# Kernel tuning notes

Measured on AMD Instinct MI355X. Metric: run time of the kernel, lower is better.

Reference implementation:

```python
import jax, jax.numpy as jnp
import numpy as np

TOP_K = 2
NUM_EXPERTS = 64
TEMPERATURE = 3.0           # buffer initial value (moe_routing_temperature default)
LOAD_BALANCE_ALPHA = 0.01
Z_LOSS_ALPHA = 1e-4


def setup_inputs() -> dict:
    key = jax.random.key(0)
    k1, k2 = jax.random.split(key)
    B, S, H, E = 4, 4096, 4096, NUM_EXPERTS
    x = jax.random.normal(k1, (B, S, H), dtype=jnp.float32)
    gate_w = jax.random.normal(k2, (E, H), dtype=jnp.float32) * (1.0 / np.sqrt(H))
    expert_bias = jnp.zeros((E,), dtype=jnp.float32)
    return {"x": x, "gate_w": gate_w, "expert_bias": expert_bias}


def reference(x, gate_w, expert_bias):
    # Eval-mode path: no noise, no warmup scaling, static top_k, seq_len < 8192
    # -> logits scaled by the temperature buffer.
    B, S, H = x.shape
    E = gate_w.shape[0]
    x_flat = x.reshape(-1, H)                               # [T, H], T = B*S
    logits = jnp.einsum('th,eh->te', x_flat, gate_w) + expert_bias  # [T, E]
    logits = logits / TEMPERATURE
    probs = jax.nn.softmax(logits, axis=-1)                 # [T, E]
    top_scores, top_idx = jax.lax.top_k(probs, TOP_K)       # [T, K]
    top_scores = top_scores / jnp.sum(top_scores, axis=-1, keepdims=True)
    # Load-balance aux loss: fraction of routed tokens per expert * mean prob.
    sel_counts = jax.nn.one_hot(top_idx, E, dtype=logits.dtype).sum(axis=1)  # [T, E]
    frac_routed = sel_counts.mean(axis=0)                   # [E], sums to TOP_K
    mean_prob = probs.mean(axis=0)                          # [E]
    lb_loss = LOAD_BALANCE_ALPHA * E * jnp.sum(frac_routed * mean_prob)
    # Z-loss for routing stability.
    z_loss = Z_LOSS_ALPHA * jnp.mean(jax.nn.logsumexp(logits, axis=-1) ** 2)
    total_loss = lb_loss + z_loss
    return top_scores, top_idx, total_loss
```

## Files before the change

kernel.cpp:

```cpp
#include <hip/hip_runtime.h>
#include <hip/hip_bf16.h>
#include <math.h>

typedef float f32x4 __attribute__((ext_vector_type(4)));

#define H_DIM   4096
#define E_EXP   64
#define NTOK    16384
#define BT      64
#define BK      64
#define LDX     68
#define NBLK    (NTOK/BT)
#define PART_STRIDE 132

__global__ __launch_bounds__(256) void moe_gate_main(
    const float* __restrict__ x, const float* __restrict__ gw,
    const float* __restrict__ bias, float* __restrict__ out,
    float* __restrict__ part)
{
    __shared__ float xs[BT * LDX];
    __shared__ float ws[E_EXP * LDX];
    __shared__ float bs[E_EXP];
    __shared__ float rs[BT];
    __shared__ int   ia[BT], ib[BT];

    const int tid  = threadIdx.x;
    const int bid  = blockIdx.x;
    const int tok0 = bid * BT;
    const int tx   = tid & 15;
    const int ty   = tid >> 4;

    if (tid < E_EXP) bs[tid] = bias[tid];

    const int srow = tid >> 4;
    const int scol = (tid & 15) * 4;
    const float* xp = x  + (size_t)(tok0 + srow) * H_DIM + scol;
    const float* wp = gw + (size_t)srow * H_DIM + scol;

    float acc[4][4];
#pragma unroll
    for (int i = 0; i < 4; i++)
#pragma unroll
        for (int j = 0; j < 4; j++) acc[i][j] = 0.f;

    f32x4 rx[4], rw[4];
#pragma unroll
    for (int i = 0; i < 4; i++) {
        rx[i] = *(const f32x4*)(xp + (size_t)(16 * i) * H_DIM);
        rw[i] = *(const f32x4*)(wp + (size_t)(16 * i) * H_DIM);
    }

    for (int c = 0; c < H_DIM / BK; c++) {
        __syncthreads();
#pragma unroll
        for (int i = 0; i < 4; i++) {
            *(f32x4*)&xs[(srow + 16 * i) * LDX + scol] = rx[i];
            *(f32x4*)&ws[(srow + 16 * i) * LDX + scol] = rw[i];
        }
        __syncthreads();
        if (c + 1 < H_DIM / BK) {
            const int k0 = (c + 1) * BK;
#pragma unroll
            for (int i = 0; i < 4; i++) {
                rx[i] = *(const f32x4*)(xp + (size_t)(16 * i) * H_DIM + k0);
                rw[i] = *(const f32x4*)(wp + (size_t)(16 * i) * H_DIM + k0);
            }
        }
#pragma unroll
        for (int kk = 0; kk < BK; kk += 4) {
            f32x4 xv[4], wv[4];
#pragma unroll
            for (int i = 0; i < 4; i++) xv[i] = *(const f32x4*)&xs[(ty + 16 * i) * LDX + kk];
#pragma unroll
            for (int j = 0; j < 4; j++) wv[j] = *(const f32x4*)&ws[(tx + 16 * j) * LDX + kk];
#pragma unroll
            for (int i = 0; i < 4; i++)
#pragma unroll
                for (int j = 0; j < 4; j++)
#pragma unroll
                    for (int q = 0; q < 4; q++)
                        acc[i][j] += xv[i][q] * wv[j][q];
        }
    }

    __syncthreads();
#pragma unroll
    for (int i = 0; i < 4; i++)
#pragma unroll
        for (int j = 0; j < 4; j++)
            xs[(ty + 16 * i) * LDX + (tx + 16 * j)] = acc[i][j];
    __syncthreads();

    float zsq = 0.f;
    if (tid < BT) {
        const float invTemp = (1.0f / 3.0f);
        float m = -1e30f, m2 = -1e30f;
        int i1 = 0, i2 = 0;
        for (int e = 0; e < E_EXP; e++) {
            float v = (xs[tid * LDX + e] + bs[e]) * invTemp;
            xs[tid * LDX + e] = v;
            if (v > m)       { m2 = m; i2 = i1; m = v; i1 = e; }
            else if (v > m2) { m2 = v; i2 = e; }
        }
        float s = 0.f;
        for (int e = 0; e < E_EXP; e++) {
            float p = expf(xs[tid * LDX + e] - m);
            xs[tid * LDX + e] = p;
            s += p;
        }
        rs[tid] = 1.0f / s;
        ia[tid] = i1; ib[tid] = i2;

        float p2   = expf(m2 - m);
        float inv12 = 1.0f / (1.0f + p2);
        out[(size_t)(tok0 + tid) * 2 + 0] = inv12;
        out[(size_t)(tok0 + tid) * 2 + 1] = p2 * inv12;
        out[(size_t)NTOK * 2 + (size_t)(tok0 + tid) * 2 + 0] = (float)i1;
        out[(size_t)NTOK * 2 + (size_t)(tok0 + tid) * 2 + 1] = (float)i2;

        float lse = m + logf(s);
        zsq = lse * lse;
#pragma unroll
        for (int o = 32; o; o >>= 1) zsq += __shfl_xor(zsq, o);
    }
    __syncthreads();

    if (tid < E_EXP) {
        float psum = 0.f, csum = 0.f;
        for (int t = 0; t < BT; t++) {
            psum += xs[t * LDX + tid] * rs[t];
            csum += (ia[t] == tid ? 1.f : 0.f) + (ib[t] == tid ? 1.f : 0.f);
        }
        part[bid * PART_STRIDE + tid]      = psum;
        part[bid * PART_STRIDE + 64 + tid] = csum;
        if (tid == 0) part[bid * PART_STRIDE + 128] = zsq;
    }
}

__global__ void moe_gate_loss(const float* __restrict__ part, float* __restrict__ out)
{
    const int tid = threadIdx.x;
    float sp = 0.f, sc = 0.f, zp = 0.f;
    for (int b = 0; b < NBLK; b++) {
        sp += part[b * PART_STRIDE + tid];
        sc += part[b * PART_STRIDE + 64 + tid];
    }
    for (int m = 0; m < NBLK / 64; m++)
        zp += part[(tid + 64 * m) * PART_STRIDE + 128];

    const float invN = 1.0f / (float)NTOK;
    float dot = (sc * invN) * (sp * invN);
#pragma unroll
    for (int o = 32; o; o >>= 1) {
        dot += __shfl_xor(dot, o);
        zp  += __shfl_xor(zp, o);
    }
    if (tid == 0)
        out[(size_t)NTOK * 4] = 0.01f * 64.0f * dot + 1e-4f * zp * invN;
}

extern "C" void kernel_launch(void* const* d_in, const int* in_sizes, int n_in,
                              void* d_out, int out_size, void* d_ws, size_t ws_size,
                              hipStream_t stream)
{
    const float* x    = (const float*)d_in[0];
    const float* gw   = (const float*)d_in[1];
    const float* bias = (const float*)d_in[2];
    float* out  = (float*)d_out;
    float* part = (float*)d_ws;

    moe_gate_main<<<NBLK, 256, 0, stream>>>(x, gw, bias, out, part);
    moe_gate_loss<<<1, 64, 0, stream>>>(part, out);
}
```

Baseline: 477.4 us.

## Replace FP32 SIMT gate GEMM with split-bf16 MFMA emulation and parallel loss reduce

Replaces the scalar FP32 tiled GEMM with bf16 MFMA instructions. Each fp32 operand is split into three bf16 parts and six cross products are accumulated to approximate fp32 accuracy. A pre-kernel splits the gate weights into bf16 planes. The main kernel now uses 16-token blocks split-K across four waves with a shared-memory reduction, runs softmax/top-2 on four lanes per token, and the final loss reduction uses 1024 threads. The aim is to move the compute-bound matmul onto matrix cores at the cost of extra split arithmetic, more weight traffic, and slightly different rounding.

```diff
diff --git a/kernel.cpp b/kernel.cpp
--- a/kernel.cpp
+++ b/kernel.cpp
@@ -3,160 +3,200 @@
 #include <math.h>
 
 typedef float f32x4 __attribute__((ext_vector_type(4)));
-
-#define H_DIM   4096
-#define E_EXP   64
-#define NTOK    16384
-#define BT      64
-#define BK      64
-#define LDX     68
-#define NBLK    (NTOK/BT)
-#define PART_STRIDE 132
+typedef short bf16x8 __attribute__((ext_vector_type(8)));
+
+#define H_DIM 4096
+#define E_EXP 64
+#define NTOK  16384
+#define PLANE (E_EXP * H_DIM)
+#define PS    132
+#define NB2   1024
+
+__device__ __forceinline__ void split8(f32x4 a, f32x4 b, bf16x8 &h, bf16x8 &m, bf16x8 &l){
+#pragma unroll
+    for (int j = 0; j < 8; j++){
+        float v = (j < 4) ? a[j] : b[j - 4];
+        __hip_bfloat16 hb = __float2bfloat16(v);
+        float r1 = v - __bfloat162float(hb);
+        __hip_bfloat16 mb = __float2bfloat16(r1);
+        float r2 = r1 - __bfloat162float(mb);
+        __hip_bfloat16 lb = __float2bfloat16(r2);
+        h[j] = __builtin_bit_cast(short, hb);
+        m[j] = __builtin_bit_cast(short, mb);
+        l[j] = __builtin_bit_cast(short, lb);
+    }
+}
+
+#define MFMA __builtin_amdgcn_mfma_f32_16x16x32_bf16
+
+__global__ __launch_bounds__(256) void moe_wsplit(
+    const float* __restrict__ gw, short* __restrict__ wpl)
+{
+    const int idx = (blockIdx.x * 256 + threadIdx.x) * 8;
+    f32x4 a = *(const f32x4*)(gw + idx);
+    f32x4 b = *(const f32x4*)(gw + idx + 4);
+    bf16x8 h, m, l; split8(a, b, h, m, l);
+    *(bf16x8*)(wpl + idx)             = h;
+    *(bf16x8*)(wpl + PLANE + idx)     = m;
+    *(bf16x8*)(wpl + 2 * PLANE + idx) = l;
+}
 
 __global__ __launch_bounds__(256) void moe_gate_main(
-    const float* __restrict__ x, const float* __restrict__ gw,
+    const float* __restrict__ x, const short* __restrict__ wpl,
     const float* __restrict__ bias, float* __restrict__ out,
     float* __restrict__ part)
 {
-    __shared__ float xs[BT * LDX];
-    __shared__ float ws[E_EXP * LDX];
-    __shared__ float bs[E_EXP];
-    __shared__ float rs[BT];
-    __shared__ int   ia[BT], ib[BT];
-
-    const int tid  = threadIdx.x;
-    const int bid  = blockIdx.x;
-    const int tok0 = bid * BT;
-    const int tx   = tid & 15;
-    const int ty   = tid >> 4;
-
-    if (tid < E_EXP) bs[tid] = bias[tid];
-
-    const int srow = tid >> 4;
-    const int scol = (tid & 15) * 4;
-    const float* xp = x  + (size_t)(tok0 + srow) * H_DIM + scol;
-    const float* wp = gw + (size_t)srow * H_DIM + scol;
-
-    float acc[4][4];
-#pragma unroll
-    for (int i = 0; i < 4; i++)
-#pragma unroll
-        for (int j = 0; j < 4; j++) acc[i][j] = 0.f;
-
-    f32x4 rx[4], rw[4];
-#pragma unroll
-    for (int i = 0; i < 4; i++) {
-        rx[i] = *(const f32x4*)(xp + (size_t)(16 * i) * H_DIM);
-        rw[i] = *(const f32x4*)(wp + (size_t)(16 * i) * H_DIM);
-    }
-
-    for (int c = 0; c < H_DIM / BK; c++) {
-        __syncthreads();
-#pragma unroll
-        for (int i = 0; i < 4; i++) {
-            *(f32x4*)&xs[(srow + 16 * i) * LDX + scol] = rx[i];
-            *(f32x4*)&ws[(srow + 16 * i) * LDX + scol] = rw[i];
-        }
-        __syncthreads();
-        if (c + 1 < H_DIM / BK) {
-            const int k0 = (c + 1) * BK;
-#pragma unroll
-            for (int i = 0; i < 4; i++) {
-                rx[i] = *(const f32x4*)(xp + (size_t)(16 * i) * H_DIM + k0);
-                rw[i] = *(const f32x4*)(wp + (size_t)(16 * i) * H_DIM + k0);
-            }
-        }
-#pragma unroll
-        for (int kk = 0; kk < BK; kk += 4) {
-            f32x4 xv[4], wv[4];
-#pragma unroll
-            for (int i = 0; i < 4; i++) xv[i] = *(const f32x4*)&xs[(ty + 16 * i) * LDX + kk];
-#pragma unroll
-            for (int j = 0; j < 4; j++) wv[j] = *(const f32x4*)&ws[(tx + 16 * j) * LDX + kk];
-#pragma unroll
-            for (int i = 0; i < 4; i++)
-#pragma unroll
-                for (int j = 0; j < 4; j++)
-#pragma unroll
-                    for (int q = 0; q < 4; q++)
-                        acc[i][j] += xv[i][q] * wv[j][q];
-        }
-    }
-
+    __shared__ f32x4 red[4][4][64];
+    __shared__ float ls[16 * 68];
+    __shared__ float bs[64], rs[16];
+    __shared__ int   ia[16], ib[16];
+
+    const int tid = threadIdx.x, bid = blockIdx.x;
+    const int wv = tid >> 6, l = tid & 63, l16 = l & 15, lk = l >> 4;
+    const int tok0 = bid * 16;
+
+    if (tid < 64) bs[tid] = bias[tid];
+
+    const float* xp = x   + (size_t)(tok0 + l16) * H_DIM + wv * 1024 + lk * 8;
+    const short* wp = wpl + l16 * H_DIM + wv * 1024 + lk * 8;
+
+    f32x4 acc[4] = {};
+
+    f32x4 xa = *(const f32x4*)xp;
+    f32x4 xb = *(const f32x4*)(xp + 4);
+
+    for (int cc = 0; cc < 32; ++cc){
+        bf16x8 xh, xm, xl; split8(xa, xb, xh, xm, xl);
+        if (cc < 31){
+            xa = *(const f32x4*)(xp + (cc + 1) * 32);
+            xb = *(const f32x4*)(xp + (cc + 1) * 32 + 4);
+        }
+        bf16x8 wf[4][3];
+#pragma unroll
+        for (int g = 0; g < 4; ++g){
+            const short* wpg = wp + g * 16 * H_DIM + cc * 32;
+#pragma unroll
+            for (int p = 0; p < 3; ++p)
+                wf[g][p] = *(const bf16x8*)(wpg + p * PLANE);
+        }
+#pragma unroll
+        for (int g = 0; g < 4; ++g){
+            acc[g] = MFMA(xh, wf[g][0], acc[g], 0, 0, 0);
+            acc[g] = MFMA(xm, wf[g][0], acc[g], 0, 0, 0);
+            acc[g] = MFMA(xh, wf[g][1], acc[g], 0, 0, 0);
+            acc[g] = MFMA(xm, wf[g][1], acc[g], 0, 0, 0);
+            acc[g] = MFMA(xh, wf[g][2], acc[g], 0, 0, 0);
+            acc[g] = MFMA(xl, wf[g][0], acc[g], 0, 0, 0);
+        }
+    }
+
+#pragma unroll
+    for (int g = 0; g < 4; ++g) red[wv][g][l] = acc[g];
     __syncthreads();
-#pragma unroll
-    for (int i = 0; i < 4; i++)
-#pragma unroll
-        for (int j = 0; j < 4; j++)
-            xs[(ty + 16 * i) * LDX + (tx + 16 * j)] = acc[i][j];
+    {
+        const int g = tid >> 6, ll = tid & 63;
+        f32x4 s = red[0][g][ll];
+#pragma unroll
+        for (int w2 = 1; w2 < 4; ++w2) s += red[w2][g][ll];
+        const int l16b = ll & 15, lkb = ll >> 4;
+#pragma unroll
+        for (int r = 0; r < 4; ++r)
+            ls[(lkb * 4 + r) * 68 + g * 16 + l16b] = s[r];
+    }
     __syncthreads();
 
-    float zsq = 0.f;
-    if (tid < BT) {
+    if (tid < 64){
+        const int t = tid >> 2, s4 = tid & 3, eb = s4 * 16;
         const float invTemp = (1.0f / 3.0f);
-        float m = -1e30f, m2 = -1e30f;
-        int i1 = 0, i2 = 0;
-        for (int e = 0; e < E_EXP; e++) {
-            float v = (xs[tid * LDX + e] + bs[e]) * invTemp;
-            xs[tid * LDX + e] = v;
-            if (v > m)       { m2 = m; i2 = i1; m = v; i1 = e; }
-            else if (v > m2) { m2 = v; i2 = e; }
-        }
-        float s = 0.f;
-        for (int e = 0; e < E_EXP; e++) {
-            float p = expf(xs[tid * LDX + e] - m);
-            xs[tid * LDX + e] = p;
-            s += p;
-        }
-        rs[tid] = 1.0f / s;
-        ia[tid] = i1; ib[tid] = i2;
-
-        float p2   = expf(m2 - m);
-        float inv12 = 1.0f / (1.0f + p2);
-        out[(size_t)(tok0 + tid) * 2 + 0] = inv12;
-        out[(size_t)(tok0 + tid) * 2 + 1] = p2 * inv12;
-        out[(size_t)NTOK * 2 + (size_t)(tok0 + tid) * 2 + 0] = (float)i1;
-        out[(size_t)NTOK * 2 + (size_t)(tok0 + tid) * 2 + 1] = (float)i2;
-
-        float lse = m + logf(s);
-        zsq = lse * lse;
+        float m1 = -1e30f, m2 = -1e30f; int i1 = 0, i2 = 0;
+        for (int j = 0; j < 16; ++j){
+            const int e = eb + j;
+            float v = (ls[t * 68 + e] + bs[e]) * invTemp;
+            ls[t * 68 + e] = v;
+            if (v > m1)      { m2 = m1; i2 = i1; m1 = v; i1 = e; }
+            else if (v > m2) { m2 = v;  i2 = e; }
+        }
+#pragma unroll
+        for (int off = 1; off <= 2; off <<= 1){
+            float om1 = __shfl_xor(m1, off), om2 = __shfl_xor(m2, off);
+            int   oi1 = __shfl_xor(i1, off), oi2 = __shfl_xor(i2, off);
+            bool sw = (om1 > m1) || (om1 == m1 && oi1 < i1);
+            float n1 = sw ? om1 : m1;  int ni1 = sw ? oi1 : i1;
+            float lm = sw ? m1  : om1; int li  = sw ? i1  : oi1;
+            float w2 = sw ? om2 : m2;  int wi  = sw ? oi2 : i2;
+            bool s2 = (lm > w2) || (lm == w2 && li < wi);
+            m1 = n1; i1 = ni1;
+            m2 = s2 ? lm : w2; i2 = s2 ? li : wi;
+        }
+        float ssum = 0.f;
+        for (int j = 0; j < 16; ++j){
+            const int e = eb + j;
+            float p = __expf(ls[t * 68 + e] - m1);
+            ls[t * 68 + e] = p;
+            ssum += p;
+        }
+        ssum += __shfl_xor(ssum, 1);
+        ssum += __shfl_xor(ssum, 2);
+
+        float zsq = 0.f;
+        if (s4 == 0){
+            rs[t] = 1.0f / ssum; ia[t] = i1; ib[t] = i2;
+            float p2    = __expf(m2 - m1);
+            float inv12 = 1.0f / (1.0f + p2);
+            out[(size_t)(tok0 + t) * 2 + 0] = inv12;
+            out[(size_t)(tok0 + t) * 2 + 1] = p2 * inv12;
+            out[(size_t)NTOK * 2 + (size_t)(tok0 + t) * 2 + 0] = (float)i1;
+            out[(size_t)NTOK * 2 + (size_t)(tok0 + t) * 2 + 1] = (float)i2;
+            float lse = m1 + logf(ssum);
+            zsq = lse * lse;
+        }
 #pragma unroll
         for (int o = 32; o; o >>= 1) zsq += __shfl_xor(zsq, o);
-    }
+
+        float psum = 0.f, csum = 0.f;
+        for (int t2 = 0; t2 < 16; ++t2){
+            psum += ls[t2 * 68 + tid] * rs[t2];
+            csum += (ia[t2] == tid ? 1.f : 0.f) + (ib[t2] == tid ? 1.f : 0.f);
+        }
+        part[bid * PS + tid]      = psum;
+        part[bid * PS + 64 + tid] = csum;
+        if (tid == 0) part[bid * PS + 128] = zsq;
+    }
+}
+
+__global__ __launch_bounds__(1024) void moe_gate_loss(
+    const float* __restrict__ part, float* __restrict__ out)
+{
+    __shared__ float spS[16][64], scS[16][64], zW[16];
+    const int tid = threadIdx.x;
+    const int e = tid & 63, g = tid >> 6;
+    float sp = 0.f, sc = 0.f;
+    for (int b = g; b < NB2; b += 16){
+        sp += part[b * PS + e];
+        sc += part[b * PS + 64 + e];
+    }
+    spS[g][e] = sp; scS[g][e] = sc;
+    float z = part[tid * PS + 128];
+#pragma unroll
+    for (int o = 32; o; o >>= 1) z += __shfl_xor(z, o);
+    if ((tid & 63) == 0) zW[g] = z;
     __syncthreads();
 
-    if (tid < E_EXP) {
-        float psum = 0.f, csum = 0.f;
-        for (int t = 0; t < BT; t++) {
-            psum += xs[t * LDX + tid] * rs[t];
-            csum += (ia[t] == tid ? 1.f : 0.f) + (ib[t] == tid ? 1.f : 0.f);
-        }
-        part[bid * PART_STRIDE + tid]      = psum;
-        part[bid * PART_STRIDE + 64 + tid] = csum;
-        if (tid == 0) part[bid * PART_STRIDE + 128] = zsq;
-    }
-}
-
-__global__ void moe_gate_loss(const float* __restrict__ part, float* __restrict__ out)
-{
-    const int tid = threadIdx.x;
-    float sp = 0.f, sc = 0.f, zp = 0.f;
-    for (int b = 0; b < NBLK; b++) {
-        sp += part[b * PART_STRIDE + tid];
-        sc += part[b * PART_STRIDE + 64 + tid];
-    }
-    for (int m = 0; m < NBLK / 64; m++)
-        zp += part[(tid + 64 * m) * PART_STRIDE + 128];
-
-    const float invN = 1.0f / (float)NTOK;
-    float dot = (sc * invN) * (sp * invN);
-#pragma unroll
-    for (int o = 32; o; o >>= 1) {
-        dot += __shfl_xor(dot, o);
-        zp  += __shfl_xor(zp, o);
-    }
-    if (tid == 0)
-        out[(size_t)NTOK * 4] = 0.01f * 64.0f * dot + 1e-4f * zp * invN;
+    if (tid < 64){
+        float tsp = 0.f, tsc = 0.f;
+#pragma unroll
+        for (int q = 0; q < 16; ++q){ tsp += spS[q][tid]; tsc += scS[q][tid]; }
+        float zp = (tid < 16) ? zW[tid] : 0.f;
+        const float invN = 1.0f / (float)NTOK;
+        float dot = (tsc * invN) * (tsp * invN);
+#pragma unroll
+        for (int o = 32; o; o >>= 1){
+            dot += __shfl_xor(dot, o);
+            zp  += __shfl_xor(zp, o);
+        }
+        if (tid == 0)
+            out[(size_t)NTOK * 4] = 0.01f * 64.0f * dot + 1e-4f * zp * invN;
+    }
 }
 
 extern "C" void kernel_launch(void* const* d_in, const int* in_sizes, int n_in,
@@ -166,9 +206,12 @@
     const float* x    = (const float*)d_in[0];
     const float* gw   = (const float*)d_in[1];
     const float* bias = (const float*)d_in[2];
-    float* out  = (float*)d_out;
-    float* part = (float*)d_ws;
-
-    moe_gate_main<<<NBLK, 256, 0, stream>>>(x, gw, bias, out, part);
-    moe_gate_loss<<<1, 64, 0, stream>>>(part, out);
-}
+    float* out = (float*)d_out;
+
+    short* wpl = (short*)d_ws;
+    float* part = (float*)((char*)d_ws + 3 * PLANE * sizeof(short));
+
+    moe_wsplit<<<128, 256, 0, stream>>>(gw, wpl);
+    moe_gate_main<<<NB2, 256, 0, stream>>>(x, wpl, bias, out, part);
+    moe_gate_loss<<<1, 1024, 0, stream>>>(part, out);
+}
```

New measurement: 542.0 us. +13.5%, slower.
